# Kernel tuning notes

Hardware: AMD Instinct MI355X
Metric: run time of the kernel (lower is better)

## Reference

```python
import jax, jax.numpy as jnp
import numpy as np

N_NODE = 200000
EMB = 64
N_EDGES = 2000000
LAYERS = 3
EPS_NORM = 1e-12


def setup_inputs() -> dict:
    key = jax.random.key(0)
    ks = jax.random.split(key, 13)
    d = EMB
    return {
        "user_emb": jax.random.normal(ks[0], (N_NODE, d), jnp.float32),
        "W0": jax.random.normal(ks[1], (d, d), jnp.float32) * np.float32(np.sqrt(2.0 / d)),
        "b0": jax.random.normal(ks[2], (1, d), jnp.float32) * 0.1,
        "W1": jax.random.normal(ks[3], (d, d), jnp.float32) * np.float32(np.sqrt(2.0 / d)),
        "b1": jax.random.normal(ks[4], (1, d), jnp.float32) * 0.1,
        "att": jax.random.normal(ks[5], (1, d), jnp.float32) * 0.1,
        "att_m": jax.random.normal(ks[6], (d, d), jnp.float32) * np.float32(np.sqrt(2.0 / d)),
        "item_rows": jax.random.randint(ks[7], (N_EDGES,), 0, N_NODE, jnp.int32),
        "item_cols": jax.random.randint(ks[8], (N_EDGES,), 0, N_NODE, jnp.int32),
        "item_vals": jax.random.uniform(ks[9], (N_EDGES,), jnp.float32),
        "user_rows": jax.random.randint(ks[10], (N_EDGES,), 0, N_NODE, jnp.int32),
        "user_cols": jax.random.randint(ks[11], (N_EDGES,), 0, N_NODE, jnp.int32),
        "user_vals": jax.random.uniform(ks[12], (N_EDGES,), jnp.float32),
    }


def _spmm(rows, cols, vals, x):
    # y[i] = sum_{edges (i,j)} vals * x[j]   (torch.sparse.mm equivalent)
    gathered = vals[:, None] * x[cols]  # [E, d]
    return jax.ops.segment_sum(gathered, rows, num_segments=N_NODE)


def _l2norm_rows(x):
    # F.normalize(x, p=2, dim=1)
    n = jnp.sqrt(jnp.sum(x * x, axis=1, keepdims=True))
    return x / jnp.maximum(n, EPS_NORM)


def _self_gating(em, W, b):
    return em * jax.nn.sigmoid(em @ W + b)


def _propagate(rows, cols, vals, u):
    acc = u
    for _ in range(LAYERS):
        u = _spmm(rows, cols, vals, u)
        acc = acc + _l2norm_rows(u)
    return acc


def reference(user_emb, W0, b0, W1, b1, att, att_m,
              item_rows, item_cols, item_vals,
              user_rows, user_cols, user_vals):
    u_c2 = _self_gating(user_emb, W0, b0)
    u_c3 = _self_gating(user_emb, W1, b1)
    e2 = _propagate(item_rows, item_cols, item_vals, u_c2)  # [N, d]
    e3 = _propagate(user_rows, user_cols, user_vals, u_c3)  # [N, d]
    # channel attention: per-node scalar score for each channel
    w2 = jnp.sum(att * (e2 @ att_m), axis=1)  # [N]
    w3 = jnp.sum(att * (e3 @ att_m), axis=1)  # [N]
    score = jax.nn.softmax(jnp.stack([w2, w3], axis=1), axis=-1)  # [N, 2]
    mixed = score[:, 0:1] * e2 + score[:, 1:2] * e3  # [N, d]
    return mixed, score
```

## Files before the change

kernel.cpp:

```cpp
#include <hip/hip_runtime.h>

#define N_NODE 200000
#define EMB 64
#define N_EDGES 2000000
#define NROWS_TOTAL (2 * N_NODE)
#define TOT_E (2 * N_EDGES)

#define BSHIFT 9
#define BROWS 512
#define NBUCK ((NROWS_TOTAL + BROWS - 1) / BROWS)
#define NB 1024
#define CHUNK ((TOT_E + NB - 1) / NB)
#define SCAN_N (NBUCK * NB)
#define MAXH 6144

#define GATE_NPB 64

typedef unsigned short bfu;

__device__ __forceinline__ float bf2f(bfu u) { return __uint_as_float(((unsigned)u) << 16); }
__device__ __forceinline__ bfu f2bf(float f) {
    unsigned b = __float_as_uint(f);
    return (bfu)((b + 0x7FFF + ((b >> 16) & 1)) >> 16);
}

__global__ void gate_kernel(const float* __restrict__ emb,
                            const float* __restrict__ W,
                            const float* __restrict__ b,
                            bfu* __restrict__ out) {
    __shared__ float4 Wl4[64][16];
    __shared__ float4 bl4[16];
    __shared__ float rowbuf[4][4][72];
    int t = threadIdx.x;
    const float4* Wg4 = (const float4*)W;
    for (int idx = t; idx < 1024; idx += 256) Wl4[idx >> 4][idx & 15] = Wg4[idx];
    if (t < 16) bl4[t] = ((const float4*)b)[t];
    __syncthreads();
    int w = t >> 6, lane = t & 63, sub = lane >> 4, l16 = lane & 15;
    int base = blockIdx.x * GATE_NPB + w * 4;
    const float4* emb4 = (const float4*)emb;
#pragma unroll 1
    for (int it = 0; it < GATE_NPB / 16; ++it, base += 16) {
        int i = base + sub;
        float4 xr = emb4[(size_t)i * 16 + l16];
        *(float4*)&rowbuf[w][sub][l16 * 4] = xr;
        __syncthreads();
        float4 s = bl4[l16];
#pragma unroll 16
        for (int k = 0; k < 64; ++k) {
            float xk = rowbuf[w][sub][k];
            float4 wv = Wl4[k][l16];
            s.x += xk * wv.x; s.y += xk * wv.y; s.z += xk * wv.z; s.w += xk * wv.w;
        }
        float4 g;
        g.x = 1.0f / (1.0f + __expf(-s.x));
        g.y = 1.0f / (1.0f + __expf(-s.y));
        g.z = 1.0f / (1.0f + __expf(-s.z));
        g.w = 1.0f / (1.0f + __expf(-s.w));
        ushort4 bv;
        bv.x = f2bf(xr.x * g.x); bv.y = f2bf(xr.y * g.y);
        bv.z = f2bf(xr.z * g.z); bv.w = f2bf(xr.w * g.w);
        ((ushort4*)out)[(size_t)i * 16 + l16] = bv;
        __syncthreads();
    }
}

__global__ void binA_kernel(const int* __restrict__ item_rows,
                            const int* __restrict__ user_rows,
                            int* __restrict__ bc) {
    __shared__ int h[NBUCK];
    int t = threadIdx.x, blk = blockIdx.x;
    for (int k = t; k < NBUCK; k += 256) h[k] = 0;
    __syncthreads();
    int lo = blk * CHUNK, hi = min(lo + CHUNK, TOT_E);
    for (int i = lo + t; i < hi; i += 256) {
        int g = (i < N_EDGES) ? item_rows[i] : (N_NODE + user_rows[i - N_EDGES]);
        atomicAdd(&h[g >> BSHIFT], 1);
    }
    __syncthreads();
    for (int k = t; k < NBUCK; k += 256) bc[k * NB + blk] = h[k];
}

__global__ void scan1_kernel(const int* __restrict__ bc, int* __restrict__ bsumP,
                             int* __restrict__ btot) {
    int b = blockIdx.x, t = threadIdx.x;
    int base = b * NB + t * 4;
    int sR = 0, sP = 0;
#pragma unroll
    for (int k = 0; k < 4; ++k) {
        int c = bc[base + k];
        sR += c;
        sP += (c + 7) & ~7;
    }
#pragma unroll
    for (int off = 32; off; off >>= 1) {
        sR += __shfl_xor(sR, off);
        sP += __shfl_xor(sP, off);
    }
    __shared__ int wsR[4], wsP[4];
    int lane = t & 63, w = t >> 6;
    if (lane == 0) { wsR[w] = sR; wsP[w] = sP; }
    __syncthreads();
    if (t == 0) {
        btot[b] = wsR[0] + wsR[1] + wsR[2] + wsR[3];
        bsumP[b] = wsP[0] + wsP[1] + wsP[2] + wsP[3];
    }
}

__global__ void scan2_kernel(const int* __restrict__ bsumP, const int* __restrict__ btot,
                             int* __restrict__ boffP, int* __restrict__ bbase) {
    __shared__ int sh[1024];
    int t = threadIdx.x;
    int vP = (t < NBUCK) ? bsumP[t] : 0;
    sh[t] = vP;
    __syncthreads();
    for (int off = 1; off < 1024; off <<= 1) {
        int u = (t >= off) ? sh[t - off] : 0;
        __syncthreads();
        sh[t] += u;
        __syncthreads();
    }
    if (t < NBUCK) boffP[t] = sh[t] - vP;
    if (t == 1023) boffP[NBUCK] = sh[1023];
    __syncthreads();
    int vR = (t < NBUCK) ? btot[t] : 0;
    sh[t] = vR;
    __syncthreads();
    for (int off = 1; off < 1024; off <<= 1) {
        int u = (t >= off) ? sh[t - off] : 0;
        __syncthreads();
        sh[t] += u;
        __syncthreads();
    }
    if (t < NBUCK) bbase[t] = sh[t] - vR;
}

__global__ void scan3_kernel(const int* __restrict__ bc, const int* __restrict__ boffP,
                             int* __restrict__ soffP) {
    int b = blockIdx.x, t = threadIdx.x;
    int lane = t & 63, w = t >> 6;
    int base = b * NB + t * 4;
    int p[4];
#pragma unroll
    for (int k = 0; k < 4; ++k) p[k] = (bc[base + k] + 7) & ~7;
    int e1 = p[0], e2 = p[0] + p[1], e3 = p[0] + p[1] + p[2];
    int tsum = e3 + p[3];
    int incl = tsum;
#pragma unroll
    for (int off = 1; off < 64; off <<= 1) {
        int u = __shfl_up(incl, off);
        if (lane >= off) incl += u;
    }
    int excl = incl - tsum;
    __shared__ int wsum[4];
    if (lane == 63) wsum[w] = incl;
    __syncthreads();
    int woff = 0;
    for (int k = 0; k < 4; ++k) if (k < w) woff += wsum[k];
    int g = boffP[b] + woff + excl;
    soffP[base + 0] = g;
    soffP[base + 1] = g + e1;
    soffP[base + 2] = g + e2;
    soffP[base + 3] = g + e3;
}

__global__ void binB_kernel(const int* __restrict__ item_rows, const int* __restrict__ item_cols,
                            const float* __restrict__ item_vals,
                            const int* __restrict__ user_rows, const int* __restrict__ user_cols,
                            const float* __restrict__ user_vals,
                            const int* __restrict__ soffP, int2* __restrict__ staged) {
    __shared__ int2 ebuf[CHUNK];
    __shared__ unsigned short sbk[CHUNK];
    __shared__ int lhist[NBUCK];
    __shared__ int lbase[NBUCK + 1];
    __shared__ int lcur[NBUCK];
    __shared__ int gb[NBUCK];
    __shared__ int wsum[4];
    int t = threadIdx.x, blk = blockIdx.x;
    for (int k = t; k < NBUCK; k += 256) {
        lhist[k] = 0;
        gb[k] = soffP[k * NB + blk];
    }
    __syncthreads();
    int lo = blk * CHUNK, hi = min(lo + CHUNK, TOT_E);
    int cnt = hi - lo;
    for (int i = lo + t; i < hi; i += 256) {
        int g = (i < N_EDGES) ? item_rows[i] : (N_NODE + user_rows[i - N_EDGES]);
        atomicAdd(&lhist[g >> BSHIFT], 1);
    }
    __syncthreads();
    {
        int i0 = t * 4;
        int p0 = (i0 < NBUCK) ? lhist[i0] : 0;
        int p1 = (i0 + 1 < NBUCK) ? lhist[i0 + 1] : 0;
        int p2 = (i0 + 2 < NBUCK) ? lhist[i0 + 2] : 0;
        int p3 = (i0 + 3 < NBUCK) ? lhist[i0 + 3] : 0;
        int tsum = p0 + p1 + p2 + p3;
        int lane = t & 63, w = t >> 6;
        int incl = tsum;
#pragma unroll
        for (int off = 1; off < 64; off <<= 1) {
            int u = __shfl_up(incl, off);
            if (lane >= off) incl += u;
        }
        if (lane == 63) wsum[w] = incl;
        __syncthreads();
        int woff = 0;
        for (int k = 0; k < w; ++k) woff += wsum[k];
        int excl = woff + incl - tsum;
        if (i0 < NBUCK) { lbase[i0] = excl; lcur[i0] = excl; }
        if (i0 + 1 < NBUCK) { lbase[i0 + 1] = excl + p0; lcur[i0 + 1] = excl + p0; }
        if (i0 + 2 < NBUCK) { lbase[i0 + 2] = excl + p0 + p1; lcur[i0 + 2] = excl + p0 + p1; }
        if (i0 + 3 < NBUCK) { lbase[i0 + 3] = excl + p0 + p1 + p2; lcur[i0 + 3] = excl + p0 + p1 + p2; }
        if (t == 255) lbase[NBUCK] = excl + tsum;
    }
    __syncthreads();
    for (int i = lo + t; i < hi; i += 256) {
        int g, c; float v;
        if (i < N_EDGES) { g = item_rows[i]; c = item_cols[i]; v = item_vals[i]; }
        else { int j = i - N_EDGES; g = N_NODE + user_rows[j]; c = user_cols[j]; v = user_vals[j]; }
        int bk = g >> BSHIFT;
        int s = atomicAdd(&lcur[bk], 1);
        ebuf[s] = make_int2(((g & (BROWS - 1)) << 18) | c, __float_as_int(v));
        sbk[s] = (unsigned short)bk;
    }
    __syncthreads();
    for (int j = t; j < cnt; j += 256) {
        int k = sbk[j];
        staged[gb[k] + (j - lbase[k])] = ebuf[j];
    }
    for (int k = t; k < NBUCK; k += 256) {
        int c = lhist[k];
        int s = gb[k] + c, e = gb[k] + ((c + 7) & ~7);
        for (int q = s; q < e; ++q) staged[q] = make_int2(-1, 0);
    }
}

__global__ void finalize_kernel(const int2* __restrict__ staged, const int* __restrict__ boffP,
                                const int* __restrict__ bbase,
                                int* __restrict__ row_ptr, int2* __restrict__ ecv) {
    __shared__ int hist[BROWS];
    __shared__ int start[BROWS + 1];
    __shared__ int2 ebuf[MAXH];
    __shared__ int wsum[4];
    int b = blockIdx.x, t = threadIdx.x;
    int base = boffP[b], end = boffP[b + 1];
    int ebase = bbase[b];
    hist[t * 2] = 0; hist[t * 2 + 1] = 0;
    __syncthreads();
    for (int k = base + t; k < end; k += 256) {
        int gx = staged[k].x;
        if (gx >= 0) atomicAdd(&hist[gx >> 18], 1);
    }
    __syncthreads();
    int i0 = t * 2;
    int c0 = hist[i0], c1 = hist[i0 + 1];
    int tsum = c0 + c1;
    int lane = t & 63, w = t >> 6;
    int incl = tsum;
#pragma unroll
    for (int off = 1; off < 64; off <<= 1) {
        int u = __shfl_up(incl, off);
        if (lane >= off) incl += u;
    }
    if (lane == 63) wsum[w] = incl;
    __syncthreads();
    int woff = 0;
    for (int k = 0; k < w; ++k) woff += wsum[k];
    int excl = woff + incl - tsum;
    start[i0] = excl; start[i0 + 1] = excl + c0;
    if (t == 255) start[BROWS] = excl + tsum;
    __syncthreads();
    int tot = start[BROWS];
#pragma unroll
    for (int q = 0; q < 2; ++q) {
        int r = i0 + q;
        int g = (b << BSHIFT) + r;
        if (g < NROWS_TOTAL) row_ptr[g] = ebase + start[r];
    }
    if (b == 0 && t == 0) row_ptr[NROWS_TOTAL] = TOT_E;
    if (tot <= MAXH) {
        hist[i0] = start[i0]; hist[i0 + 1] = start[i0 + 1];
        __syncthreads();
        for (int k = base + t; k < end; k += 256) {
            int2 p = staged[k];
            if (p.x < 0) continue;
            int l = atomicAdd(&hist[p.x >> 18], 1);
            ebuf[l] = make_int2(p.x & 0x3FFFF, p.y);
        }
        __syncthreads();
        for (int j = t; j < tot; j += 256) ecv[ebase + j] = ebuf[j];
    } else {
        hist[i0] = ebase + start[i0]; hist[i0 + 1] = ebase + start[i0 + 1];
        __syncthreads();
        for (int k = base + t; k < end; k += 256) {
            int2 p = staged[k];
            if (p.x < 0) continue;
            int pos = atomicAdd(&hist[p.x >> 18], 1);
            ecv[pos] = make_int2(p.x & 0x3FFFF, p.y);
        }
    }
}

__global__ void spmm_y(const int* __restrict__ row_ptr, const int2* __restrict__ ecv,
                       const bfu* __restrict__ x,
                       bfu* __restrict__ y, float* __restrict__ rinv, int n) {
    int t = threadIdx.x;
    int lane = t & 63;
    int sub = lane >> 4;
    int l16 = lane & 15;
    int i = blockIdx.x * 16 + (t >> 6) * 4 + sub;
    if (i >= n) return;
    int s = row_ptr[i], e = row_ptr[i + 1];
    const ushort4* x4 = (const ushort4*)x;
    float4 a = make_float4(0.f, 0.f, 0.f, 0.f);
    int gbase = sub * 16;
    for (int base = s; base < e; base += 16) {
        int idx = base + l16;
        int cl = 0; float vl = 0.0f;
        if (idx < e) { int2 p = ecv[idx]; cl = p.x; vl = __int_as_float(p.y); }
        int cnt = min(16, e - base);
        int cnt4 = (cnt + 3) & ~3;
        for (int k = 0; k < cnt4; k += 4) {
#pragma unroll
            for (int u = 0; u < 4; ++u) {
                int c = __shfl(cl, gbase + k + u);
                float v = __shfl(vl, gbase + k + u);
                ushort4 xv = x4[(size_t)c * 16 + l16];
                a.x += v * bf2f(xv.x); a.y += v * bf2f(xv.y);
                a.z += v * bf2f(xv.z); a.w += v * bf2f(xv.w);
            }
        }
    }
    size_t o4 = (size_t)i * 16 + l16;
    ushort4 bv;
    bv.x = f2bf(a.x); bv.y = f2bf(a.y); bv.z = f2bf(a.z); bv.w = f2bf(a.w);
    ((ushort4*)y)[o4] = bv;
    float sq = a.x * a.x + a.y * a.y + a.z * a.z + a.w * a.w;
#pragma unroll
    for (int off = 8; off; off >>= 1) sq += __shfl_xor(sq, off);
    if (l16 == 0) rinv[i] = 1.0f / fmaxf(sqrtf(sq), 1e-12f);
}

__global__ void spmm_sum(const int* __restrict__ row_ptr, const int2* __restrict__ ecv,
                         const bfu* __restrict__ x ,
                         const bfu* __restrict__ u0, const bfu* __restrict__ y1,
                         const float* __restrict__ r1, const float* __restrict__ r2,
                         float* __restrict__ mixed, int n) {
    int t = threadIdx.x;
    int lane = t & 63;
    int sub = lane >> 4;
    int l16 = lane & 15;
    int i = blockIdx.x * 16 + (t >> 6) * 4 + sub;
    if (i >= n) return;
    int s = row_ptr[i], e = row_ptr[i + 1];
    const ushort4* x4 = (const ushort4*)x;
    float4 a = make_float4(0.f, 0.f, 0.f, 0.f);
    int gbase = sub * 16;
    for (int base = s; base < e; base += 16) {
        int idx = base + l16;
        int cl = 0; float vl = 0.0f;
        if (idx < e) { int2 p = ecv[idx]; cl = p.x; vl = __int_as_float(p.y); }
        int cnt = min(16, e - base);
        int cnt4 = (cnt + 3) & ~3;
        for (int k = 0; k < cnt4; k += 4) {
#pragma unroll
            for (int u = 0; u < 4; ++u) {
                int c = __shfl(cl, gbase + k + u);
                float v = __shfl(vl, gbase + k + u);
                ushort4 xv = x4[(size_t)c * 16 + l16];
                a.x += v * bf2f(xv.x); a.y += v * bf2f(xv.y);
                a.z += v * bf2f(xv.z); a.w += v * bf2f(xv.w);
            }
        }
    }
    float sq = a.x * a.x + a.y * a.y + a.z * a.z + a.w * a.w;
#pragma unroll
    for (int off = 8; off; off >>= 1) sq += __shfl_xor(sq, off);
    float r3 = 1.0f / fmaxf(sqrtf(sq), 1e-12f);
    size_t o4 = (size_t)i * 16 + l16;
    float a1 = r1[i], a2 = r2[i];
    ushort4 b0 = ((const ushort4*)u0)[o4];
    ushort4 b1 = ((const ushort4*)y1)[o4];
    ushort4 b2 = ((const ushort4*)x)[o4];
    float4 o;
    o.x = bf2f(b0.x) + a1 * bf2f(b1.x) + a2 * bf2f(b2.x) + r3 * a.x;
    o.y = bf2f(b0.y) + a1 * bf2f(b1.y) + a2 * bf2f(b2.y) + r3 * a.y;
    o.z = bf2f(b0.z) + a1 * bf2f(b1.z) + a2 * bf2f(b2.z) + r3 * a.z;
    o.w = bf2f(b0.w) + a1 * bf2f(b1.w) + a2 * bf2f(b2.w) + r3 * a.w;
    ((float4*)mixed)[o4] = o;
}

__global__ void spmm_mix(const int* __restrict__ row_ptr, const int2* __restrict__ ecv,
                         const bfu* __restrict__ x ,
                         const bfu* __restrict__ u0, const bfu* __restrict__ y1,
                         const float* __restrict__ r1, const float* __restrict__ r2,
                         float* __restrict__ mixed, const float* __restrict__ vvec,
                         float* __restrict__ score, int n) {
    int t = threadIdx.x;
    int lane = t & 63;
    int sub = lane >> 4;
    int l16 = lane & 15;
    int i = blockIdx.x * 16 + (t >> 6) * 4 + sub;
    if (i >= n) return;
    int s = row_ptr[i], e = row_ptr[i + 1];
    const ushort4* x4 = (const ushort4*)x;
    float4 a = make_float4(0.f, 0.f, 0.f, 0.f);
    int gbase = sub * 16;
    for (int base = s; base < e; base += 16) {
        int idx = base + l16;
        int cl = 0; float vl = 0.0f;
        if (idx < e) { int2 p = ecv[idx]; cl = p.x; vl = __int_as_float(p.y); }
        int cnt = min(16, e - base);
        int cnt4 = (cnt + 3) & ~3;
        for (int k = 0; k < cnt4; k += 4) {
#pragma unroll
            for (int u = 0; u < 4; ++u) {
                int c = __shfl(cl, gbase + k + u);
                float v = __shfl(vl, gbase + k + u);
                ushort4 xv = x4[(size_t)c * 16 + l16];
                a.x += v * bf2f(xv.x); a.y += v * bf2f(xv.y);
                a.z += v * bf2f(xv.z); a.w += v * bf2f(xv.w);
            }
        }
    }
    float sq = a.x * a.x + a.y * a.y + a.z * a.z + a.w * a.w;
#pragma unroll
    for (int off = 8; off; off >>= 1) sq += __shfl_xor(sq, off);
    float r3 = 1.0f / fmaxf(sqrtf(sq), 1e-12f);
    size_t o4 = (size_t)i * 16 + l16;
    float a1 = r1[i], a2s = r2[i];
    ushort4 b0 = ((const ushort4*)u0)[o4];
    ushort4 b1 = ((const ushort4*)y1)[o4];
    ushort4 b2 = ((const ushort4*)x)[o4];
    float4 a3;
    a3.x = bf2f(b0.x) + a1 * bf2f(b1.x) + a2s * bf2f(b2.x) + r3 * a.x;
    a3.y = bf2f(b0.y) + a1 * bf2f(b1.y) + a2s * bf2f(b2.y) + r3 * a.y;
    a3.z = bf2f(b0.z) + a1 * bf2f(b1.z) + a2s * bf2f(b2.z) + r3 * a.z;
    a3.w = bf2f(b0.w) + a1 * bf2f(b1.w) + a2s * bf2f(b2.w) + r3 * a.w;
    float4 a2 = ((float4*)mixed)[o4];
    float4 vv = ((const float4*)vvec)[l16];
    float w2 = a2.x * vv.x + a2.y * vv.y + a2.z * vv.z + a2.w * vv.w;
    float w3 = a3.x * vv.x + a3.y * vv.y + a3.z * vv.z + a3.w * vv.w;
#pragma unroll
    for (int off = 8; off; off >>= 1) {
        w2 += __shfl_xor(w2, off);
        w3 += __shfl_xor(w3, off);
    }
    float m = fmaxf(w2, w3);
    float x2 = __expf(w2 - m), x3 = __expf(w3 - m);
    float inv = 1.0f / (x2 + x3);
    float s2 = x2 * inv, s3 = x3 * inv;
    float4 o;
    o.x = s2 * a2.x + s3 * a3.x; o.y = s2 * a2.y + s3 * a3.y;
    o.z = s2 * a2.z + s3 * a3.z; o.w = s2 * a2.w + s3 * a3.w;
    ((float4*)mixed)[o4] = o;
    if (l16 == 0) { score[(size_t)i * 2] = s2; score[(size_t)i * 2 + 1] = s3; }
}

__global__ void vvec_kernel(const float* __restrict__ att_m, const float* __restrict__ att,
                            float* __restrict__ v) {
    int k = threadIdx.x;
    float s = 0.0f;
    for (int j = 0; j < 64; ++j) s += att_m[k * 64 + j] * att[j];
    v[k] = s;
}

extern "C" void kernel_launch(void* const* d_in, const int* in_sizes, int n_in,
                              void* d_out, int out_size, void* d_ws, size_t ws_size,
                              hipStream_t stream) {
    const float* user_emb = (const float*)d_in[0];
    const float* W0 = (const float*)d_in[1];
    const float* b0 = (const float*)d_in[2];
    const float* W1 = (const float*)d_in[3];
    const float* b1 = (const float*)d_in[4];
    const float* att = (const float*)d_in[5];
    const float* att_m = (const float*)d_in[6];
    const int* item_rows = (const int*)d_in[7];
    const int* item_cols = (const int*)d_in[8];
    const float* item_vals = (const float*)d_in[9];
    const int* user_rows = (const int*)d_in[10];
    const int* user_cols = (const int*)d_in[11];
    const float* user_vals = (const float*)d_in[12];

    float* out = (float*)d_out;
    float* mixed = out;
    float* score = out + (size_t)N_NODE * 64;

    char* w = (char*)d_ws;
    bfu* u0 = (bfu*)w;         w += (size_t)N_NODE * 64 * 2;
    bfu* y1 = (bfu*)w;         w += (size_t)N_NODE * 64 * 2;
    bfu* y2 = (bfu*)w;         w += (size_t)N_NODE * 64 * 2;
    float* rv1 = (float*)w;    w += (size_t)N_NODE * 4;
    float* rv2 = (float*)w;    w += (size_t)N_NODE * 4;
    int* row_ptr = (int*)w;    w += ((size_t)NROWS_TOTAL + 64) * 4;
    int2* ecv = (int2*)w;      w += (size_t)TOT_E * 8;
    float* vvec = (float*)w;   w += 256;
    int* bc = (int*)w;         w += (size_t)SCAN_N * 4;
    int* soffP = (int*)w;      w += (size_t)SCAN_N * 4;
    int* bsumP = (int*)w;      w += (NBUCK + 8) * 4;
    int* btot = (int*)w;       w += (NBUCK + 8) * 4;
    int* boffP = (int*)w;      w += (NBUCK + 8) * 4;
    int* bbase = (int*)w;      w += (NBUCK + 8) * 4;
    int2* staged = (int2*)u0;

    const int NB16 = (N_NODE + 15) / 16;
    const int GATE_B = N_NODE / GATE_NPB;
    const int* rp_item = row_ptr;
    const int* rp_user = row_ptr + N_NODE;

    binA_kernel<<<NB, 256, 0, stream>>>(item_rows, user_rows, bc);
    scan1_kernel<<<NBUCK, 256, 0, stream>>>(bc, bsumP, btot);
    scan2_kernel<<<1, 1024, 0, stream>>>(bsumP, btot, boffP, bbase);
    scan3_kernel<<<NBUCK, 256, 0, stream>>>(bc, boffP, soffP);
    binB_kernel<<<NB, 256, 0, stream>>>(item_rows, item_cols, item_vals,
                                        user_rows, user_cols, user_vals, soffP, staged);
    finalize_kernel<<<NBUCK, 256, 0, stream>>>(staged, boffP, bbase, row_ptr, ecv);
    vvec_kernel<<<1, 64, 0, stream>>>(att_m, att, vvec);

    gate_kernel<<<GATE_B, 256, 0, stream>>>(user_emb, W0, b0, u0);
    spmm_y<<<NB16, 256, 0, stream>>>(rp_item, ecv, u0, y1, rv1, N_NODE);
    spmm_y<<<NB16, 256, 0, stream>>>(rp_item, ecv, y1, y2, rv2, N_NODE);
    spmm_sum<<<NB16, 256, 0, stream>>>(rp_item, ecv, y2, u0, y1, rv1, rv2, mixed, N_NODE);

    gate_kernel<<<GATE_B, 256, 0, stream>>>(user_emb, W1, b1, u0);
    spmm_y<<<NB16, 256, 0, stream>>>(rp_user, ecv, u0, y1, rv1, N_NODE);
    spmm_y<<<NB16, 256, 0, stream>>>(rp_user, ecv, y1, y2, rv2, N_NODE);
    spmm_mix<<<NB16, 256, 0, stream>>>(rp_user, ecv, y2, u0, y1, rv1, rv2,
                                       mixed, vvec, score, N_NODE);
}
```

Measured before the change: 492.8 us.

## Use bf16 MFMA for gating matmul and reuse binA bucket counts in binB

The self-gating matmul now runs on bf16 MFMA 16x16x32 instructions, with W held in registers, in place of scalar FMA loops over shared-memory weights. binB no longer rebuilds its per-block bucket histogram from the row arrays and reads the counts binA already wrote. This removes a full pass over the row indices and replaces the gate kernel's FP32 scalar arithmetic with matrix-core work. The trade-off is that the gate matmul inputs are rounded to bf16, and the epilogue re-reads emb with a strided scalar access pattern.

```diff
diff --git a/kernel.cpp b/kernel.cpp
--- a/kernel.cpp
+++ b/kernel.cpp
@@ -14,9 +14,9 @@
 #define SCAN_N (NBUCK * NB)
 #define MAXH 6144
 
-#define GATE_NPB 64
-
 typedef unsigned short bfu;
+typedef __attribute__((ext_vector_type(8))) short bf16x8;
+typedef __attribute__((ext_vector_type(4))) float f32x4;
 
 __device__ __forceinline__ float bf2f(bfu u) { return __uint_as_float(((unsigned)u) << 16); }
 __device__ __forceinline__ bfu f2bf(float f) {
@@ -27,41 +27,61 @@
 __global__ void gate_kernel(const float* __restrict__ emb,
                             const float* __restrict__ W,
                             const float* __restrict__ b,
-                            bfu* __restrict__ out) {
-    __shared__ float4 Wl4[64][16];
-    __shared__ float4 bl4[16];
-    __shared__ float rowbuf[4][4][72];
+                            bfu* __restrict__ out, int n) {
     int t = threadIdx.x;
-    const float4* Wg4 = (const float4*)W;
-    for (int idx = t; idx < 1024; idx += 256) Wl4[idx >> 4][idx & 15] = Wg4[idx];
-    if (t < 16) bl4[t] = ((const float4*)b)[t];
-    __syncthreads();
-    int w = t >> 6, lane = t & 63, sub = lane >> 4, l16 = lane & 15;
-    int base = blockIdx.x * GATE_NPB + w * 4;
-    const float4* emb4 = (const float4*)emb;
+    int w = t >> 6, lane = t & 63;
+    int l16 = lane & 15, kg = lane >> 4;
+    bf16x8 Bf[2][4];
+#pragma unroll
+    for (int kb = 0; kb < 2; ++kb)
+#pragma unroll
+        for (int nt = 0; nt < 4; ++nt) {
+            bf16x8 f;
+#pragma unroll
+            for (int e = 0; e < 8; ++e)
+                f[e] = (short)f2bf(W[(kb * 32 + kg * 8 + e) * 64 + nt * 16 + l16]);
+            Bf[kb][nt] = f;
+        }
+    float bias[4];
+#pragma unroll
+    for (int nt = 0; nt < 4; ++nt) bias[nt] = b[nt * 16 + l16];
+    const float4* e4 = (const float4*)emb;
 #pragma unroll 1
-    for (int it = 0; it < GATE_NPB / 16; ++it, base += 16) {
-        int i = base + sub;
-        float4 xr = emb4[(size_t)i * 16 + l16];
-        *(float4*)&rowbuf[w][sub][l16 * 4] = xr;
-        __syncthreads();
-        float4 s = bl4[l16];
-#pragma unroll 16
-        for (int k = 0; k < 64; ++k) {
-            float xk = rowbuf[w][sub][k];
-            float4 wv = Wl4[k][l16];
-            s.x += xk * wv.x; s.y += xk * wv.y; s.z += xk * wv.z; s.w += xk * wv.w;
-        }
-        float4 g;
-        g.x = 1.0f / (1.0f + __expf(-s.x));
-        g.y = 1.0f / (1.0f + __expf(-s.y));
-        g.z = 1.0f / (1.0f + __expf(-s.z));
-        g.w = 1.0f / (1.0f + __expf(-s.w));
-        ushort4 bv;
-        bv.x = f2bf(xr.x * g.x); bv.y = f2bf(xr.y * g.y);
-        bv.z = f2bf(xr.z * g.z); bv.w = f2bf(xr.w * g.w);
-        ((ushort4*)out)[(size_t)i * 16 + l16] = bv;
-        __syncthreads();
+    for (int it = 0; it < 4; ++it) {
+        int tile = blockIdx.x * 16 + w * 4 + it;
+        if (tile * 16 >= n) break;
+        int arow = tile * 16 + l16;
+        size_t ab = (size_t)arow * 16 + kg * 2;
+        float4 a0 = e4[ab], a1 = e4[ab + 1];
+        float4 a2 = e4[ab + 8], a3 = e4[ab + 9];
+        bf16x8 A0, A1;
+        A0[0] = (short)f2bf(a0.x); A0[1] = (short)f2bf(a0.y);
+        A0[2] = (short)f2bf(a0.z); A0[3] = (short)f2bf(a0.w);
+        A0[4] = (short)f2bf(a1.x); A0[5] = (short)f2bf(a1.y);
+        A0[6] = (short)f2bf(a1.z); A0[7] = (short)f2bf(a1.w);
+        A1[0] = (short)f2bf(a2.x); A1[1] = (short)f2bf(a2.y);
+        A1[2] = (short)f2bf(a2.z); A1[3] = (short)f2bf(a2.w);
+        A1[4] = (short)f2bf(a3.x); A1[5] = (short)f2bf(a3.y);
+        A1[6] = (short)f2bf(a3.z); A1[7] = (short)f2bf(a3.w);
+        f32x4 acc[4];
+#pragma unroll
+        for (int nt = 0; nt < 4; ++nt) {
+            acc[nt] = (f32x4){0.f, 0.f, 0.f, 0.f};
+            acc[nt] = __builtin_amdgcn_mfma_f32_16x16x32_bf16(A0, Bf[0][nt], acc[nt], 0, 0, 0);
+            acc[nt] = __builtin_amdgcn_mfma_f32_16x16x32_bf16(A1, Bf[1][nt], acc[nt], 0, 0, 0);
+        }
+#pragma unroll
+        for (int nt = 0; nt < 4; ++nt) {
+#pragma unroll
+            for (int r = 0; r < 4; ++r) {
+                int orow = tile * 16 + kg * 4 + r;
+                int col = nt * 16 + l16;
+                float s = acc[nt][r] + bias[nt];
+                float g = 1.0f / (1.0f + __expf(-s));
+                float xv = emb[(size_t)orow * 64 + col];
+                out[(size_t)orow * 64 + col] = f2bf(xv * g);
+            }
+        }
     }
 }
 
@@ -168,33 +188,22 @@
                             const float* __restrict__ item_vals,
                             const int* __restrict__ user_rows, const int* __restrict__ user_cols,
                             const float* __restrict__ user_vals,
-                            const int* __restrict__ soffP, int2* __restrict__ staged) {
+                            const int* __restrict__ bc, const int* __restrict__ soffP,
+                            int2* __restrict__ staged) {
     __shared__ int2 ebuf[CHUNK];
     __shared__ unsigned short sbk[CHUNK];
-    __shared__ int lhist[NBUCK];
     __shared__ int lbase[NBUCK + 1];
     __shared__ int lcur[NBUCK];
     __shared__ int gb[NBUCK];
     __shared__ int wsum[4];
     int t = threadIdx.x, blk = blockIdx.x;
-    for (int k = t; k < NBUCK; k += 256) {
-        lhist[k] = 0;
-        gb[k] = soffP[k * NB + blk];
-    }
-    __syncthreads();
-    int lo = blk * CHUNK, hi = min(lo + CHUNK, TOT_E);
-    int cnt = hi - lo;
-    for (int i = lo + t; i < hi; i += 256) {
-        int g = (i < N_EDGES) ? item_rows[i] : (N_NODE + user_rows[i - N_EDGES]);
-        atomicAdd(&lhist[g >> BSHIFT], 1);
-    }
-    __syncthreads();
+    for (int k = t; k < NBUCK; k += 256) gb[k] = soffP[k * NB + blk];
     {
         int i0 = t * 4;
-        int p0 = (i0 < NBUCK) ? lhist[i0] : 0;
-        int p1 = (i0 + 1 < NBUCK) ? lhist[i0 + 1] : 0;
-        int p2 = (i0 + 2 < NBUCK) ? lhist[i0 + 2] : 0;
-        int p3 = (i0 + 3 < NBUCK) ? lhist[i0 + 3] : 0;
+        int p0 = (i0 < NBUCK) ? bc[i0 * NB + blk] : 0;
+        int p1 = (i0 + 1 < NBUCK) ? bc[(i0 + 1) * NB + blk] : 0;
+        int p2 = (i0 + 2 < NBUCK) ? bc[(i0 + 2) * NB + blk] : 0;
+        int p3 = (i0 + 3 < NBUCK) ? bc[(i0 + 3) * NB + blk] : 0;
         int tsum = p0 + p1 + p2 + p3;
         int lane = t & 63, w = t >> 6;
         int incl = tsum;
@@ -215,6 +224,8 @@
         if (t == 255) lbase[NBUCK] = excl + tsum;
     }
     __syncthreads();
+    int lo = blk * CHUNK, hi = min(lo + CHUNK, TOT_E);
+    int cnt = hi - lo;
     for (int i = lo + t; i < hi; i += 256) {
         int g, c; float v;
         if (i < N_EDGES) { g = item_rows[i]; c = item_cols[i]; v = item_vals[i]; }
@@ -230,7 +241,7 @@
         staged[gb[k] + (j - lbase[k])] = ebuf[j];
     }
     for (int k = t; k < NBUCK; k += 256) {
-        int c = lhist[k];
+        int c = lbase[k + 1] - lbase[k];
         int s = gb[k] + c, e = gb[k] + ((c + 7) & ~7);
         for (int q = s; q < e; ++q) staged[q] = make_int2(-1, 0);
     }
@@ -505,7 +516,7 @@
     int2* staged = (int2*)u0;
 
     const int NB16 = (N_NODE + 15) / 16;
-    const int GATE_B = N_NODE / GATE_NPB;
+    const int GATE_B = (N_NODE / 16 + 15) / 16;
     const int* rp_item = row_ptr;
     const int* rp_user = row_ptr + N_NODE;
 
@@ -514,16 +525,16 @@
     scan2_kernel<<<1, 1024, 0, stream>>>(bsumP, btot, boffP, bbase);
     scan3_kernel<<<NBUCK, 256, 0, stream>>>(bc, boffP, soffP);
     binB_kernel<<<NB, 256, 0, stream>>>(item_rows, item_cols, item_vals,
-                                        user_rows, user_cols, user_vals, soffP, staged);
+                                        user_rows, user_cols, user_vals, bc, soffP, staged);
     finalize_kernel<<<NBUCK, 256, 0, stream>>>(staged, boffP, bbase, row_ptr, ecv);
     vvec_kernel<<<1, 64, 0, stream>>>(att_m, att, vvec);
 
-    gate_kernel<<<GATE_B, 256, 0, stream>>>(user_emb, W0, b0, u0);
+    gate_kernel<<<GATE_B, 256, 0, stream>>>(user_emb, W0, b0, u0, N_NODE);
     spmm_y<<<NB16, 256, 0, stream>>>(rp_item, ecv, u0, y1, rv1, N_NODE);
     spmm_y<<<NB16, 256, 0, stream>>>(rp_item, ecv, y1, y2, rv2, N_NODE);
     spmm_sum<<<NB16, 256, 0, stream>>>(rp_item, ecv, y2, u0, y1, rv1, rv2, mixed, N_NODE);
 
-    gate_kernel<<<GATE_B, 256, 0, stream>>>(user_emb, W1, b1, u0);
+    gate_kernel<<<GATE_B, 256, 0, stream>>>(user_emb, W1, b1, u0, N_NODE);
     spmm_y<<<NB16, 256, 0, stream>>>(rp_user, ecv, u0, y1, rv1, N_NODE);
     spmm_y<<<NB16, 256, 0, stream>>>(rp_user, ecv, y1, y2, rv2, N_NODE);
     spmm_mix<<<NB16, 256, 0, stream>>>(rp_user, ecv, y2, u0, y1, rv1, rv2,
```

After: 438.5 us. 11.0% less time.
